# Optimization experiments

Hardware: AMD Instinct MI355X
Metric: run time of the kernel (lower is better)

## Reference

```python
import jax, jax.numpy as jnp
import numpy as np

T, B, A = 64, 512, 5
XD, YD, ZD, HD, MD = 2, 10, 16, 200, 90
HMIC, HMAC = 200, 200


def setup_inputs() -> dict:
    key = jax.random.key(0)
    ks = jax.random.split(key, 40)
    it = iter(range(40))
    def nrm(shape, s=0.05):
        return jax.random.normal(ks[next(it)], shape, jnp.float32) * s
    inp = {}
    inp["y"] = jax.random.normal(ks[next(it)], (T, B, YD), jnp.float32)
    # values in {-1} u [0, MD): -1 means "sample macro goal"
    inp["macro_goals"] = jax.random.randint(ks[next(it)], (T, B, A), 0, MD + 1, jnp.int32) - 1
    # dec_macro: Linear(YD+HMAC,HD) ReLU Linear(HD,MD) LogSoftmax
    inp["Wdm1"] = nrm((A, YD + HMAC, HD)); inp["bdm1"] = nrm((A, HD))
    inp["Wdm2"] = nrm((A, HD, MD));        inp["bdm2"] = nrm((A, MD))
    # prior: Linear(MD+HMIC,HD) ReLU Linear(HD,HD) ReLU
    inp["Wpr1"] = nrm((A, MD + HMIC, HD)); inp["bpr1"] = nrm((A, HD))
    inp["Wpr2"] = nrm((A, HD, HD));        inp["bpr2"] = nrm((A, HD))
    inp["Wpm"] = nrm((A, HD, ZD)); inp["bpm"] = nrm((A, ZD))
    inp["Wps"] = nrm((A, HD, ZD)); inp["bps"] = nrm((A, ZD))
    # dec: Linear(YD+MD+ZD+HMIC,HD) ReLU Linear(HD,HD) ReLU
    inp["Wd1"] = nrm((A, YD + MD + ZD + HMIC, HD)); inp["bd1"] = nrm((A, HD))
    inp["Wd2"] = nrm((A, HD, HD));                  inp["bd2"] = nrm((A, HD))
    inp["Wdx"] = nrm((A, HD, XD)); inp["bdx"] = nrm((A, XD))
    inp["Wds"] = nrm((A, HD, XD)); inp["bds"] = nrm((A, XD))
    # per-agent micro GRU (input XD+ZD, hidden HMIC), torch gate order [r;z;n]
    inp["Wih_mic"] = nrm((A, 3 * HMIC, XD + ZD)); inp["Whh_mic"] = nrm((A, 3 * HMIC, HMIC))
    inp["bih_mic"] = nrm((A, 3 * HMIC));          inp["bhh_mic"] = nrm((A, 3 * HMIC))
    # macro GRU (input A*MD, hidden HMAC)
    inp["Wih_mac"] = nrm((3 * HMAC, A * MD)); inp["Whh_mac"] = nrm((3 * HMAC, HMAC))
    inp["bih_mac"] = nrm((3 * HMAC,));        inp["bhh_mac"] = nrm((3 * HMAC,))
    # pre-drawn sampling noise: gumbel for multinomial, standard normal for gaussians
    u = jax.random.uniform(ks[next(it)], (T - 1, A, B, MD), jnp.float32, 1e-6, 1.0 - 1e-6)
    inp["eps_g"] = -jnp.log(-jnp.log(u))
    inp["eps_z"] = jax.random.normal(ks[next(it)], (T - 1, A, B, ZD), jnp.float32)
    inp["eps_x"] = jax.random.normal(ks[next(it)], (T - 1, A, B, XD), jnp.float32)
    inp["burn_in"] = 8
    return inp


def reference(y, Wdm1, bdm1, Wdm2, bdm2, Wpr1, bpr1, Wpr2, bpr2, Wpm, bpm, Wps, bps,
              Wd1, bd1, Wd2, bd2, Wdx, bdx, Wds, bds,
              Wih_mic, Whh_mic, bih_mic, bhh_mic, Wih_mac, Whh_mac, bih_mac, bhh_mac,
              eps_g, eps_z, eps_x, macro_goals, burn_in):
    def lin(x, W, b):  # per-agent linear: x [A,B,I], W [A,I,O]
        return jnp.einsum('abi,aio->abo', x, W) + b[:, None]

    def gru1(x, h, Wih, Whh, bih, bhh):  # x [B,I], h [B,H]
        gi = x @ Wih.T + bih
        gh = h @ Whh.T + bhh
        ir, iz, inn = jnp.split(gi, 3, -1)
        hr, hz, hn = jnp.split(gh, 3, -1)
        r = jax.nn.sigmoid(ir + hr); zg = jax.nn.sigmoid(iz + hz)
        return (1 - zg) * jnp.tanh(inn + r * hn) + zg * h

    def gruA(x, h, Wih, Whh, bih, bhh):  # x [A,B,I], h [A,B,H]
        gi = jnp.einsum('abi,agi->abg', x, Wih) + bih[:, None]
        gh = jnp.einsum('abh,agh->abg', h, Whh) + bhh[:, None]
        ir, iz, inn = jnp.split(gi, 3, -1)
        hr, hz, hn = jnp.split(gh, 3, -1)
        r = jax.nn.sigmoid(ir + hr); zg = jax.nn.sigmoid(iz + hz)
        return (1 - zg) * jnp.tanh(inn + r * hn) + zg * h

    goals_in = macro_goals[:T - 1, 0, :]  # [T-1, A]; torch code only reads batch row 0

    def step(carry, xs):
        y_t, h_mic, h_mac = carry
        t, curr, g_t, ez_t, ex_t, y_next_true = xs
        yA = jnp.broadcast_to(y_t, (A, B, YD))
        hmacA = jnp.broadcast_to(h_mac, (A, B, HMAC))
        # macro-goal decoder (log-softmax) and goal selection
        hdm = jax.nn.relu(lin(jnp.concatenate([yA, hmacA], -1), Wdm1, bdm1))
        logp = jax.nn.log_softmax(lin(hdm, Wdm2, bdm2), -1)          # [A,B,MD]
        samp_flag = (curr == -1) | ((t >= burn_in) & (burn_in > 0))  # [A]
        sampled = jax.nn.one_hot(jnp.argmax(logp + g_t, -1), MD, dtype=logp.dtype)
        fixed = jnp.zeros((A, B, MD), logp.dtype).at[:, 0, :].set(
            jax.nn.one_hot(curr, MD, dtype=logp.dtype))  # torch sets only batch row 0
        m_t = jnp.where(samp_flag[:, None, None], sampled, fixed)    # [A,B,MD]
        goals_out = jnp.argmax(m_t, -1).T                            # [B,A]
        # macro GRU over concatenated agent goals
        h_mac2 = gru1(jnp.transpose(m_t, (1, 0, 2)).reshape(B, A * MD),
                      h_mac, Wih_mac, Whh_mac, bih_mac, bhh_mac)
        # prior -> sample z
        hp = jax.nn.relu(lin(jax.nn.relu(lin(jnp.concatenate([m_t, h_mic], -1),
                                             Wpr1, bpr1)), Wpr2, bpr2))
        z_t = lin(hp, Wpm, bpm) + jax.nn.softplus(lin(hp, Wps, bps)) * ez_t  # [A,B,ZD]
        # decoder -> sample next positions (teacher-forced during burn-in)
        hd = jax.nn.relu(lin(jax.nn.relu(lin(jnp.concatenate([yA, m_t, z_t, h_mic], -1),
                                             Wd1, bd1)), Wd2, bd2))
        x_samp = lin(hd, Wdx, bdx) + jax.nn.softplus(lin(hd, Wds, bds)) * ex_t  # [A,B,XD]
        x_true = jnp.transpose(y_next_true.reshape(B, A, XD), (1, 0, 2))
        x_next = jnp.where(t < burn_in, x_true, x_samp)
        y_next = jnp.transpose(x_next, (1, 0, 2)).reshape(B, YD)
        # per-agent micro GRUs on [x_next, z]
        h_mic2 = gruA(jnp.concatenate([x_next, z_t], -1), h_mic,
                      Wih_mic, Whh_mic, bih_mic, bhh_mic)
        return (y_next, h_mic2, h_mac2), (y_next, goals_out)

    carry0 = (y[0], jnp.zeros((A, B, HMIC), y.dtype), jnp.zeros((B, HMAC), y.dtype))
    xs = (jnp.arange(T - 1), goals_in, eps_g, eps_z, eps_x, y[1:])
    _, (ys, goals) = jax.lax.scan(step, carry0, xs)
    ret = jnp.concatenate([y[:1], ys], 0)                 # [T,B,YD]
    goals_full = jnp.concatenate([goals, goals[-1:]], 0)  # [T,B,A]; last = second-last
    return ret, goals_full
```

## Files before the change

kernel.cpp:

```cpp
#include <hip/hip_runtime.h>


#define T_STEPS 63
#define BATCH   512
#define NA      5
#define YDIM    10
#define ZDIM    16
#define XDIM    2
#define HD      200
#define MDIM    90
#define HM      200
#define NB      8
#define NT      256

struct Params {
  const float *yin;
  const int   *mg;
  const float *Wdm1,*bdm1,*bdm2;
  const float *Wpr1,*bpr1,*Wpr2,*bpr2,*Wpm,*bpm,*Wps,*bps;
  const float *Wd1,*bd1,*Wd2,*bd2,*Wdx,*bdx,*Wds,*bds;
  const float *bih_mic,*bhh_mic,*bih_mac,*bhh_mac;
  const float *eps_g,*eps_z,*eps_x;
  const int   *burn;
  const float *WihTmic,*WhhTmic,*WihTmac,*WhhTmac,*Wdm2p;
  float *hmac_ws,*hmic_ws;
  int   *idxA,*idxB;
  float *ret,*goals;
};

__device__ __forceinline__ float sigm(float x){ return 1.f/(1.f+expf(-x)); }
__device__ __forceinline__ float softplusf(float x){ return log1pf(expf(-fabsf(x))) + fmaxf(x,0.f); }

template<int NBv>
__device__ __forceinline__ void mv4(const float* __restrict__ W, int N, int K,
                                    const float* __restrict__ act, int astride,
                                    int o, int kseg, float acc[4][NBv])
{
  const int Q = K >> 2;
  const int qpt = (Q + 3) >> 2;
  int q0 = kseg * qpt;
  int q1 = (Q < q0 + qpt) ? Q : (q0 + qpt);
  for (int q = q0; q < q1; ++q) {
    const float* wr = W + (size_t)(4*q)*N + o;
    const float4 w0 = *(const float4*)(wr);
    const float4 w1 = *(const float4*)(wr + N);
    const float4 w2 = *(const float4*)(wr + 2*N);
// ... 68 lines not shown
    int a = j / 10800, r = j % 10800;
    int k = r / 600, g = r % 600;
    WihTmic[j] = Wih_mic[a*10800 + g*18 + k];
  } else if (i < 1044000) {
    int j = i - 774000;
    int k = j / 600, g = j % 600;
    WihTmac[j] = Wih_mac[g*450 + k];
  } else if (i < 1140000) {
    int j = i - 1044000;
    int a = j / 19200, r = j % 19200;
    int k = r / 96, o = r % 96;
    Wdm2p[j] = (o < 90) ? Wdm2[(a*200 + k)*90 + o] : 0.f;
  }
}

__global__ __launch_bounds__(NT, 2) void step_kernel(Params p, int t)
{
  __shared__ __align__(16) float sY[NB][12];
  __shared__ __align__(16) float sHmac[NB][208];
  __shared__ __align__(16) float sHmic[NB][208];
  __shared__ __align__(16) float sGS[NB][608];
  __shared__ __align__(16) float sHn[NB][208];
  __shared__ __align__(16) float sB1[NB][208];
  __shared__ __align__(16) float sB2[NB][208];
  __shared__ __align__(16) float sLog[NB][96];
  __shared__ __align__(16) float sZ[NB][16];
  __shared__ __align__(16) float sXC[NB][20];
  __shared__ float sRedM[NB][2][8];
  __shared__ float sRedS[NB][2][8];
  __shared__ int   sIdxP[NA][NB];
  __shared__ int   sMid[NB];

  const int tid = threadIdx.x;
  const int bid = blockIdx.x;
  const int X = bid & 7, slot = bid >> 3;
  const int jj = X * 40 + slot;
  const int a  = jj >> 6;
  const int b0 = (jj & 63) * NB;
  const int burn = p.burn[0];
  const int* idxPrev = (t & 1) ? p.idxA : p.idxB;
  int*       idxCur  = (t & 1) ? p.idxB : p.idxA;

  const int og = tid >> 2;
  const int kseg = tid & 3;

  for (int u = tid; u < NB*YDIM; u += NT) {
    int j = u / YDIM, k = u % YDIM;
    float yv = (t == 0) ? p.yin[(b0+j)*YDIM + k]
                        : p.ret[(size_t)t*BATCH*YDIM + (b0+j)*YDIM + k];
    sY[j][k] = yv;
  }
  for (int u = tid; u < NB*HM; u += NT) {
    int j = u / HM, k = u % HM;
    size_t soff = ((size_t)a*BATCH + b0 + j)*HM + k;
    sHmac[j][k] = (t <= 1) ? 0.f : p.hmac_ws[soff];
    sHmic[j][k] = (t == 0) ? 0.f : p.hmic_ws[soff];
  }
  if (tid < NA*NB) {
    int a2 = tid / NB, j = tid % NB;
    sIdxP[a2][j] = (t == 0) ? -1 : idxPrev[a2*BATCH + b0 + j];
  }
  if (t == 0 && tid < NB*XDIM) {
    int j = tid >> 1, o = tid & 1;
    p.ret[(b0+j)*YDIM + a*XDIM + o] = p.yin[(b0+j)*YDIM + a*XDIM + o];
  }
  __syncthreads();

  if (t > 0) {
    #pragma unroll 1
    for (int pass = 0; pass < 3; ++pass) {
      int g4 = og + pass*64;
      if (g4 < 150) {
        int g = g4*4;
        float aI[4][NB], aH[4][NB];
        #pragma unroll
        for (int c = 0; c < 4; ++c)
          #pragma unroll
          for (int j = 0; j < NB; ++j) { aI[c][j] = 0.f; aH[c][j] = 0.f; }
        for (int a2 = kseg; a2 < NA; a2 += 4) {
          #pragma unroll
          for (int j = 0; j < NB; ++j) {
            int r = sIdxP[a2][j];
            if (r >= 0) {
              const float4 w = *(const float4*)(p.WihTmac + (size_t)(a2*MDIM + r)*600 + g);
              aI[0][j] += w.x; aI[1][j] += w.y; aI[2][j] += w.z; aI[3][j] += w.w;
            }
          }
        }
        mv4<NB>(p.WhhTmac, 600, HM, &sHmac[0][0], 208, g, kseg, aH);
        qreduce<NB>(aI);
        qreduce<NB>(aH);
        const float4 bi = *(const float4*)(p.bih_mac + g);
        const float4 bh = *(const float4*)(p.bhh_mac + g);
        #pragma unroll
        for (int j = 0; j < NB; ++j) {
          if ((j >> 1) == kseg) {
            float i0 = aI[0][j]+bi.x, i1 = aI[1][j]+bi.y, i2 = aI[2][j]+bi.z, i3 = aI[3][j]+bi.w;
            float h0 = aH[0][j]+bh.x, h1 = aH[1][j]+bh.y, h2 = aH[2][j]+bh.z, h3 = aH[3][j]+bh.w;
            if (g < 400) {
              *(float4*)&sGS[j][g] = make_float4(i0+h0, i1+h1, i2+h2, i3+h3);
            } else {
              *(float4*)&sGS[j][g] = make_float4(i0, i1, i2, i3);
              *(float4*)&sHn[j][g-400] = make_float4(h0, h1, h2, h3);
            }
          }
        }
      }
    }
    __syncthreads();
    for (int u = tid; u < NB*HM; u += NT) {
      int j = u / HM, k = u % HM;
      float r  = sigm(sGS[j][k]);
      float zg = sigm(sGS[j][200+k]);
      float nh = (1.f - zg)*tanhf(sGS[j][400+k] + r*sHn[j][k]) + zg*sHmac[j][k];
      sHmac[j][k] = nh;
      p.hmac_ws[((size_t)a*BATCH + b0 + j)*HM + k] = nh;
    }
    __syncthreads();
  }

  if (og < 50) {
    int o = og*4;
    float acc[4][NB];
    #pragma unroll
    for (int c = 0; c < 4; ++c)
      #pragma unroll
      for (int j = 0; j < NB; ++j) acc[c][j] = 0.f;
    const float* W = p.Wdm1 + (size_t)a*(YDIM+HM)*HD;
    mv4<NB>(W, HD, YDIM, &sY[0][0], 12, o, kseg, acc);
    mv4<NB>(W + (size_t)YDIM*HD, HD, HM, &sHmac[0][0], 208, o, kseg, acc);
    qreduce<NB>(acc);
    const float4 bv = *(const float4*)(p.bdm1 + a*HD + o);
    #pragma unroll
    for (int j = 0; j < NB; ++j) {
      if ((j >> 1) == kseg) {
        *(float4*)&sB1[j][o] = make_float4(
          fmaxf(acc[0][j]+bv.x, 0.f), fmaxf(acc[1][j]+bv.y, 0.f),
          fmaxf(acc[2][j]+bv.z, 0.f), fmaxf(acc[3][j]+bv.w, 0.f));
      }
    }
  }
  __syncthreads();
  if (og < 24) {
    int o = og*4;
    float acc[4][NB];
    #pragma unroll
    for (int c = 0; c < 4; ++c)
      #pragma unroll
      for (int j = 0; j < NB; ++j) acc[c][j] = 0.f;
    mv4<NB>(p.Wdm2p + (size_t)a*HD*96, 96, HD, &sB1[0][0], 208, o, kseg, acc);
    qreduce<NB>(acc);
    float b0v = (o+0 < MDIM) ? p.bdm2[a*MDIM + o+0] : 0.f;
    float b1v = (o+1 < MDIM) ? p.bdm2[a*MDIM + o+1] : 0.f;
    float b2v = (o+2 < MDIM) ? p.bdm2[a*MDIM + o+2] : 0.f;
    float b3v = (o+3 < MDIM) ? p.bdm2[a*MDIM + o+3] : 0.f;
    #pragma unroll
    for (int j = 0; j < NB; ++j) {
      if ((j >> 1) == kseg) {
        *(float4*)&sLog[j][o] = make_float4(acc[0][j]+b0v, acc[1][j]+b1v,
                                            acc[2][j]+b2v, acc[3][j]+b3v);
      }
    }
  }
  __syncthreads();
  for (int u = tid; u < NB*MDIM; u += NT) {
    int j = u / MDIM, cc = u % MDIM;
    sLog[j][cc] += p.eps_g[(((size_t)t*NA + a)*BATCH + b0 + j)*MDIM + cc];
  }
  __syncthreads();
  if (tid < NB) {
    int j = tid;
    float best = sLog[j][0]; int bi = 0;
    for (int cc = 1; cc < MDIM; ++cc) { float v = sLog[j][cc]; if (v > best) { best = v; bi = cc; } }
    int curr = p.mg[(size_t)t*BATCH*NA + a];
    bool sf = (curr == -1) || ((t >= burn) && (burn > 0));
    int mi = sf ? bi : ((b0 + j) == 0 ? curr : -1);
    sMid[j] = mi;
    float gv = (float)(mi < 0 ? 0 : mi);
    p.goals[(size_t)t*BATCH*NA + (b0+j)*NA + a] = gv;
    if (t == T_STEPS-1) p.goals[(size_t)T_STEPS*BATCH*NA + (b0+j)*NA + a] = gv;
    idxCur[a*BATCH + b0 + j] = mi;
  }
  __syncthreads();

  if (og < 50) {
    int o = og*4;
    float acc[4][NB];
    #pragma unroll
    for (int c = 0; c < 4; ++c)
      #pragma unroll
      for (int j = 0; j < NB; ++j) acc[c][j] = 0.f;
    const float* W = p.Wpr1 + (size_t)a*(MDIM+HM)*HD;
    #pragma unroll
    for (int j = 0; j < NB; ++j) {
      if ((j >> 1) == kseg) {
        int mi = sMid[j];
        if (mi >= 0) {
          const float4 w = *(const float4*)(W + (size_t)mi*HD + o);
          acc[0][j] += w.x; acc[1][j] += w.y; acc[2][j] += w.z; acc[3][j] += w.w;
        }
      }
    }
    mv4<NB>(W + (size_t)MDIM*HD, HD, HM, &sHmic[0][0], 208, o, kseg, acc);
    qreduce<NB>(acc);
    const float4 bv = *(const float4*)(p.bpr1 + a*HD + o);
    #pragma unroll
    for (int j = 0; j < NB; ++j) {
      if ((j >> 1) == kseg) {
        *(float4*)&sB2[j][o] = make_float4(
          fmaxf(acc[0][j]+bv.x, 0.f), fmaxf(acc[1][j]+bv.y, 0.f),
          fmaxf(acc[2][j]+bv.z, 0.f), fmaxf(acc[3][j]+bv.w, 0.f));
      }
    }
  }
  __syncthreads();
  if (og < 50) {
    int o = og*4;
    float acc[4][NB];
    #pragma unroll
    for (int c = 0; c < 4; ++c)
      #pragma unroll
      for (int j = 0; j < NB; ++j) acc[c][j] = 0.f;
    mv4<NB>(p.Wpr2 + (size_t)a*HD*HD, HD, HD, &sB2[0][0], 208, o, kseg, acc);
    qreduce<NB>(acc);
    const float4 bv = *(const float4*)(p.bpr2 + a*HD + o);
    #pragma unroll
    for (int j = 0; j < NB; ++j) {
      if ((j >> 1) == kseg) {
        *(float4*)&sB1[j][o] = make_float4(
          fmaxf(acc[0][j]+bv.x, 0.f), fmaxf(acc[1][j]+bv.y, 0.f),
          fmaxf(acc[2][j]+bv.z, 0.f), fmaxf(acc[3][j]+bv.w, 0.f));
      }
    }
  }
  __syncthreads();
  if (tid < NB*ZDIM) {
    int j = tid >> 4, o = tid & 15;
    float am = p.bpm[a*ZDIM + o], as = p.bps[a*ZDIM + o];
    const float* wm  = p.Wpm + (size_t)a*HD*ZDIM + o;
    const float* wsp = p.Wps + (size_t)a*HD*ZDIM + o;
    for (int k = 0; k < HD; ++k) {
      float h = sB1[j][k];
      am = fmaf(h, wm[(size_t)k*ZDIM], am);
      as = fmaf(h, wsp[(size_t)k*ZDIM], as);
    }
    float zv = am + softplusf(as) * p.eps_z[(((size_t)t*NA + a)*BATCH + b0 + j)*ZDIM + o];
    sZ[j][o] = zv;
    sXC[j][2+o] = zv;
  }
  __syncthreads();

  if (og < 50) {
    int o = og*4;
    float acc[4][NB];
    #pragma unroll
    for (int c = 0; c < 4; ++c)
      #pragma unroll
      for (int j = 0; j < NB; ++j) acc[c][j] = 0.f;
    const float* W = p.Wd1 + (size_t)a*(YDIM+MDIM+ZDIM+HM)*HD;
    #pragma unroll
    for (int j = 0; j < NB; ++j) {
      if ((j >> 1) == kseg) {
        int mi = sMid[j];
        if (mi >= 0) {
          const float4 w = *(const float4*)(W + (size_t)(YDIM+mi)*HD + o);
          acc[0][j] += w.x; acc[1][j] += w.y; acc[2][j] += w.z; acc[3][j] += w.w;
        }
      }
    }
    mv4<NB>(W, HD, YDIM, &sY[0][0], 12, o, kseg, acc);
    mv4<NB>(W + (size_t)(YDIM+MDIM)*HD, HD, ZDIM, &sZ[0][0], 16, o, kseg, acc);
    mv4<NB>(W + (size_t)(YDIM+MDIM+ZDIM)*HD, HD, HM, &sHmic[0][0], 208, o, kseg, acc);
    qreduce<NB>(acc);
    const float4 bv = *(const float4*)(p.bd1 + a*HD + o);
    #pragma unroll
    for (int j = 0; j < NB; ++j) {
      if ((j >> 1) == kseg) {
        *(float4*)&sB2[j][o] = make_float4(
          fmaxf(acc[0][j]+bv.x, 0.f), fmaxf(acc[1][j]+bv.y, 0.f),
          fmaxf(acc[2][j]+bv.z, 0.f), fmaxf(acc[3][j]+bv.w, 0.f));
      }
    }
  }
  __syncthreads();
  if (og < 50) {
    int o = og*4;
    float acc[4][NB];
    #pragma unroll
    for (int c = 0; c < 4; ++c)
      #pragma unroll
      for (int j = 0; j < NB; ++j) acc[c][j] = 0.f;
    mv4<NB>(p.Wd2 + (size_t)a*HD*HD, HD, HD, &sB2[0][0], 208, o, kseg, acc);
    qreduce<NB>(acc);
    const float4 bv = *(const float4*)(p.bd2 + a*HD + o);
    #pragma unroll
    for (int j = 0; j < NB; ++j) {
      if ((j >> 1) == kseg) {
        *(float4*)&sB1[j][o] = make_float4(
          fmaxf(acc[0][j]+bv.x, 0.f), fmaxf(acc[1][j]+bv.y, 0.f),
          fmaxf(acc[2][j]+bv.z, 0.f), fmaxf(acc[3][j]+bv.w, 0.f));
      }
    }
  }
  __syncthreads();
  if (tid < 128) {
    int j = tid >> 4, o = (tid >> 3) & 1, seg = tid & 7;
    float am = 0.f, as = 0.f;
    const float* wx  = p.Wdx + (size_t)a*HD*XDIM + o;
    const float* wsd = p.Wds + (size_t)a*HD*XDIM + o;
    for (int k = seg*25; k < seg*25 + 25; ++k) {
      float h = sB1[j][k];
      am = fmaf(h, wx[(size_t)k*XDIM], am);
      as = fmaf(h, wsd[(size_t)k*XDIM], as);
    }
    sRedM[j][o][seg] = am; sRedS[j][o][seg] = as;
  }
  __syncthreads();
  if (tid < NB*XDIM) {
    int j = tid >> 1, o = tid & 1;
    float am = p.bdx[a*XDIM + o], as = p.bds[a*XDIM + o];
    for (int s2 = 0; s2 < 8; ++s2) { am += sRedM[j][o][s2]; as += sRedS[j][o][s2]; }
    float xs = am + softplusf(as) * p.eps_x[(((size_t)t*NA + a)*BATCH + b0 + j)*XDIM + o];
    float xt = p.yin[((size_t)(t+1))*BATCH*YDIM + (b0+j)*YDIM + a*XDIM + o];
    float xv = (t < burn) ? xt : xs;
    p.ret[((size_t)(t+1))*BATCH*YDIM + (b0+j)*YDIM + a*XDIM + o] = xv;
    sXC[j][o] = xv;
  }
  __syncthreads();

  #pragma unroll 1
  for (int pass = 0; pass < 3; ++pass) {
    int g4 = og + pass*64;
    if (g4 < 150) {
      int g = g4*4;
      float aI[4][NB], aH[4][NB];
      #pragma unroll
      for (int c = 0; c < 4; ++c)
        #pragma unroll
        for (int j = 0; j < NB; ++j) { aI[c][j] = 0.f; aH[c][j] = 0.f; }
      mv4<NB>(p.WihTmic + (size_t)a*18*600, 600, 18, &sXC[0][0], 20, g, kseg, aI);
      mv4<NB>(p.WhhTmic + (size_t)a*HM*600, 600, HM, &sHmic[0][0], 208, g, kseg, aH);
      qreduce<NB>(aI);
      qreduce<NB>(aH);
      const float4 bi = *(const float4*)(p.bih_mic + a*600 + g);
      const float4 bh = *(const float4*)(p.bhh_mic + a*600 + g);
      #pragma unroll
      for (int j = 0; j < NB; ++j) {
        if ((j >> 1) == kseg) {
          float i0 = aI[0][j]+bi.x, i1 = aI[1][j]+bi.y, i2 = aI[2][j]+bi.z, i3 = aI[3][j]+bi.w;
          float h0 = aH[0][j]+bh.x, h1 = aH[1][j]+bh.y, h2 = aH[2][j]+bh.z, h3 = aH[3][j]+bh.w;
          if (g < 400) {
            *(float4*)&sGS[j][g] = make_float4(i0+h0, i1+h1, i2+h2, i3+h3);
          } else {
            *(float4*)&sGS[j][g] = make_float4(i0, i1, i2, i3);
            *(float4*)&sHn[j][g-400] = make_float4(h0, h1, h2, h3);
          }
        }
      }
    }
  }
  __syncthreads();
  for (int u = tid; u < NB*HM; u += NT) {
    int j = u / HM, k = u % HM;
    float r  = sigm(sGS[j][k]);
    float zg = sigm(sGS[j][200+k]);
    float nh = (1.f - zg)*tanhf(sGS[j][400+k] + r*sHn[j][k]) + zg*sHmic[j][k];
    p.hmic_ws[((size_t)a*BATCH + b0 + j)*HM + k] = nh;
  }
}

extern "C" void kernel_launch(void* const* d_in, const int* in_sizes, int n_in,
                              void* d_out, int out_size, void* d_ws, size_t ws_size,
                              hipStream_t stream) {
  (void)in_sizes; (void)n_in; (void)out_size; (void)ws_size;
  Params p;
  p.yin   = (const float*)d_in[0];
  p.mg    = (const int*)  d_in[1];
  p.Wdm1  = (const float*)d_in[2];  p.bdm1 = (const float*)d_in[3];
  const float* Wdm2 = (const float*)d_in[4];
  p.bdm2  = (const float*)d_in[5];
  p.Wpr1  = (const float*)d_in[6];  p.bpr1 = (const float*)d_in[7];
  p.Wpr2  = (const float*)d_in[8];  p.bpr2 = (const float*)d_in[9];
// ... 8 lines not shown
  p.bih_mic = (const float*)d_in[24]; p.bhh_mic = (const float*)d_in[25];
  const float* Wih_mac = (const float*)d_in[26];
  const float* Whh_mac = (const float*)d_in[27];
  p.bih_mac = (const float*)d_in[28]; p.bhh_mac = (const float*)d_in[29];
  p.eps_g = (const float*)d_in[30];
  p.eps_z = (const float*)d_in[31];
  p.eps_x = (const float*)d_in[32];
  p.burn  = (const int*)  d_in[33];

  float* ws = (float*)d_ws;
  float* WhhTmac = ws;
  float* WhhTmic = ws + 120000;
  float* WihTmic = ws + 720000;
  float* WihTmac = ws + 774000;
  float* Wdm2p   = ws + 1044000;
  p.hmac_ws = ws + 1140000;
  p.hmic_ws = ws + 1652000;
  int* idxbuf = (int*)(ws + 2164000);
  p.idxA = idxbuf;
  p.idxB = idxbuf + NA*BATCH;
  p.WhhTmac = WhhTmac; p.WhhTmic = WhhTmic; p.WihTmic = WihTmic; p.WihTmac = WihTmac;
  p.Wdm2p = Wdm2p;

  p.ret   = (float*)d_out;
  p.goals = (float*)d_out + (size_t)(T_STEPS+1)*BATCH*YDIM;

  prep_kernel<<<(1140000 + 255)/256, 256, 0, stream>>>(
      Whh_mac, Whh_mic, Wih_mic, Wih_mac, Wdm2,
      WhhTmac, WhhTmic, WihTmic, WihTmac, Wdm2p);

  for (int t = 0; t < T_STEPS; ++t)
    step_kernel<<<NA*64, NT, 0, stream>>>(p, t);
}
```

Measured before the change: 9.711 ms.

## Replace per-step launches with persistent cooperative kernel using flag-based inter-block sync

Turns the 63 per-timestep kernel launches into one persistent cooperative kernel. Blocks keep the GRU hidden states in shared memory across steps and exchange only macro-goal indices and sampled positions through small double-buffered global arrays. Each block waits on per-chunk acquire/release flags for just the five agent blocks of its batch chunk instead of a global barrier. It also folds the GRU reset gate into the gate computation so shared scratch can be unioned, and splits the z-head reduction across two threads. The cost is spin-waiting, and the design depends on all blocks being co-resident; if the cooperative launch fails it falls back to per-step launches.

```diff
diff --git a/kernel.cpp b/kernel.cpp
--- a/kernel.cpp
+++ b/kernel.cpp
@@ -12,6 +12,7 @@
 #define HM      200
 #define NB      8
 #define NT      256
+#define NCH     64
 
 struct Params {
   const float *yin;
@@ -23,13 +24,33 @@
   const float *eps_g,*eps_z,*eps_x;
   const int   *burn;
   const float *WihTmic,*WhhTmic,*WihTmac,*WhhTmac,*Wdm2p;
+  float *cx;
+  int   *cidx;
+  int   *fidx,*fy;
   float *hmac_ws,*hmic_ws;
-  int   *idxA,*idxB;
   float *ret,*goals;
 };
 
 __device__ __forceinline__ float sigm(float x){ return 1.f/(1.f+expf(-x)); }
 __device__ __forceinline__ float softplusf(float x){ return log1pf(expf(-fabsf(x))) + fmaxf(x,0.f); }
+__device__ __forceinline__ int ld_acq(const int* f){
+  return __hip_atomic_load(f, __ATOMIC_ACQUIRE, __HIP_MEMORY_SCOPE_AGENT);
+}
+__device__ __forceinline__ void st_rel(int* f, int v){
+  __hip_atomic_store(f, v, __ATOMIC_RELEASE, __HIP_MEMORY_SCOPE_AGENT);
+}
+__device__ __forceinline__ int ld_rlx(const int* q){
+  return __hip_atomic_load(q, __ATOMIC_RELAXED, __HIP_MEMORY_SCOPE_AGENT);
+}
+__device__ __forceinline__ float ld_rlxf(const float* q){
+  return __hip_atomic_load(q, __ATOMIC_RELAXED, __HIP_MEMORY_SCOPE_AGENT);
+}
+__device__ __forceinline__ void st_rlx(int* q, int v){
+  __hip_atomic_store(q, v, __ATOMIC_RELAXED, __HIP_MEMORY_SCOPE_AGENT);
+}
+__device__ __forceinline__ void st_rlxf(float* q, float v){
+  __hip_atomic_store(q, v, __ATOMIC_RELAXED, __HIP_MEMORY_SCOPE_AGENT);
+}
 
 template<int NBv>
 __device__ __forceinline__ void mv4(const float* __restrict__ W, int N, int K,
@@ -128,69 +149,106 @@
   }
 }
 
-__global__ __launch_bounds__(NT, 2) void step_kernel(Params p, int t)
+__global__ __launch_bounds__(NT, 2) void persist_kernel(Params p, int t0, int t1)
 {
-  __shared__ __align__(16) float sY[NB][12];
   __shared__ __align__(16) float sHmac[NB][208];
   __shared__ __align__(16) float sHmic[NB][208];
-  __shared__ __align__(16) float sGS[NB][608];
-  __shared__ __align__(16) float sHn[NB][208];
-  __shared__ __align__(16) float sB1[NB][208];
-  __shared__ __align__(16) float sB2[NB][208];
-  __shared__ __align__(16) float sLog[NB][96];
+  __shared__ __align__(16) float sXC[NB][20];
   __shared__ __align__(16) float sZ[NB][16];
-  __shared__ __align__(16) float sXC[NB][20];
   __shared__ float sRedM[NB][2][8];
   __shared__ float sRedS[NB][2][8];
-  __shared__ int   sIdxP[NA][NB];
-  __shared__ int   sMid[NB];
+  __shared__ __align__(16) union ScratchU {
+    float gs[NB][400];
+    struct { float b1[NB][208]; float b2[NB][208]; float lg[NB][96]; float y[NB][12]; } m;
+  } U;
+  __shared__ int sIdxP[NA][NB];
+  __shared__ int sMid[NB];
 
   const int tid = threadIdx.x;
   const int bid = blockIdx.x;
   const int X = bid & 7, slot = bid >> 3;
   const int jj = X * 40 + slot;
   const int a  = jj >> 6;
-  const int b0 = (jj & 63) * NB;
+  const int c  = jj & 63;
+  const int b0 = c * NB;
   const int burn = p.burn[0];
-  const int* idxPrev = (t & 1) ? p.idxA : p.idxB;
-  int*       idxCur  = (t & 1) ? p.idxB : p.idxA;
-
   const int og = tid >> 2;
   const int kseg = tid & 3;
 
-  for (int u = tid; u < NB*YDIM; u += NT) {
-    int j = u / YDIM, k = u % YDIM;
-    float yv = (t == 0) ? p.yin[(b0+j)*YDIM + k]
-                        : p.ret[(size_t)t*BATCH*YDIM + (b0+j)*YDIM + k];
-    sY[j][k] = yv;
-  }
-  for (int u = tid; u < NB*HM; u += NT) {
-    int j = u / HM, k = u % HM;
-    size_t soff = ((size_t)a*BATCH + b0 + j)*HM + k;
-    sHmac[j][k] = (t <= 1) ? 0.f : p.hmac_ws[soff];
-    sHmic[j][k] = (t == 0) ? 0.f : p.hmic_ws[soff];
-  }
-  if (tid < NA*NB) {
-    int a2 = tid / NB, j = tid % NB;
-    sIdxP[a2][j] = (t == 0) ? -1 : idxPrev[a2*BATCH + b0 + j];
-  }
-  if (t == 0 && tid < NB*XDIM) {
-    int j = tid >> 1, o = tid & 1;
-    p.ret[(b0+j)*YDIM + a*XDIM + o] = p.yin[(b0+j)*YDIM + a*XDIM + o];
+  if (t0 == 0) {
+    for (int u = tid; u < NB*HM; u += NT) {
+      int j = u / HM, k = u % HM;
+      sHmac[j][k] = 0.f; sHmic[j][k] = 0.f;
+    }
+    if (tid < NB*XDIM) {
+      int j = tid >> 1, o = tid & 1;
+      p.ret[(b0+j)*YDIM + a*XDIM + o] = p.yin[(b0+j)*YDIM + a*XDIM + o];
+    }
+  } else {
+    for (int u = tid; u < NB*HM; u += NT) {
+      int j = u / HM, k = u % HM;
+      size_t soff = ((size_t)a*BATCH + b0 + j)*HM + k;
+      sHmac[j][k] = p.hmac_ws[soff];
+      sHmic[j][k] = p.hmic_ws[soff];
+    }
   }
   __syncthreads();
 
-  if (t > 0) {
-    #pragma unroll 1
-    for (int pass = 0; pass < 3; ++pass) {
-      int g4 = og + pass*64;
-      if (g4 < 150) {
-        int g = g4*4;
+  for (int t = t0; t < t1; ++t) {
+    if (t > 0) {
+      if (tid < NA) {
+        int* f = &p.fidx[c*NA + tid];
+        while (ld_acq(f) < t) __builtin_amdgcn_s_sleep(1);
+      }
+      __syncthreads();
+      if (tid < NA*NB) {
+        int a2 = tid / NB, j = tid % NB;
+        sIdxP[a2][j] = ld_rlx(&p.cidx[((t-1)&1)*(NCH*NA*NB) + c*(NA*NB) + a2*NB + j]);
+      }
+      __syncthreads();
+      #pragma unroll 1
+      for (int pass = 0; pass < 2; ++pass) {
+        int gq = og + pass*64;
+        if (gq < 100) {
+          int g = gq*4;
+          float aI[4][NB], aH[4][NB];
+          #pragma unroll
+          for (int cc = 0; cc < 4; ++cc)
+            #pragma unroll
+            for (int j = 0; j < NB; ++j) { aI[cc][j] = 0.f; aH[cc][j] = 0.f; }
+          for (int a2 = kseg; a2 < NA; a2 += 4) {
+            #pragma unroll
+            for (int j = 0; j < NB; ++j) {
+              int r = sIdxP[a2][j];
+              if (r >= 0) {
+                const float4 w = *(const float4*)(p.WihTmac + (size_t)(a2*MDIM + r)*600 + g);
+                aI[0][j] += w.x; aI[1][j] += w.y; aI[2][j] += w.z; aI[3][j] += w.w;
+              }
+            }
+          }
+          mv4<NB>(p.WhhTmac, 600, HM, &sHmac[0][0], 208, g, kseg, aH);
+          qreduce<NB>(aI);
+          qreduce<NB>(aH);
+          const float4 bi = *(const float4*)(p.bih_mac + g);
+          const float4 bh = *(const float4*)(p.bhh_mac + g);
+          #pragma unroll
+          for (int j = 0; j < NB; ++j) {
+            if ((j >> 1) == kseg) {
+              *(float4*)&U.gs[j][g] = make_float4(aI[0][j]+bi.x+aH[0][j]+bh.x,
+                                                  aI[1][j]+bi.y+aH[1][j]+bh.y,
+                                                  aI[2][j]+bi.z+aH[2][j]+bh.z,
+                                                  aI[3][j]+bi.w+aH[3][j]+bh.w);
+            }
+          }
+        }
+      }
+      if (og < 50) {
+        int g = 400 + og*4, k4 = og*4;
         float aI[4][NB], aH[4][NB];
         #pragma unroll
-        for (int c = 0; c < 4; ++c)
+        for (int cc = 0; cc < 4; ++cc)
           #pragma unroll
-          for (int j = 0; j < NB; ++j) { aI[c][j] = 0.f; aH[c][j] = 0.f; }
+          for (int j = 0; j < NB; ++j) { aI[cc][j] = 0.f; aH[cc][j] = 0.f; }
         for (int a2 = kseg; a2 < NA; a2 += 4) {
           #pragma unroll
           for (int j = 0; j < NB; ++j) {
@@ -209,249 +267,305 @@
         #pragma unroll
         for (int j = 0; j < NB; ++j) {
           if ((j >> 1) == kseg) {
-            float i0 = aI[0][j]+bi.x, i1 = aI[1][j]+bi.y, i2 = aI[2][j]+bi.z, i3 = aI[3][j]+bi.w;
-            float h0 = aH[0][j]+bh.x, h1 = aH[1][j]+bh.y, h2 = aH[2][j]+bh.z, h3 = aH[3][j]+bh.w;
-            if (g < 400) {
-              *(float4*)&sGS[j][g] = make_float4(i0+h0, i1+h1, i2+h2, i3+h3);
-            } else {
-              *(float4*)&sGS[j][g] = make_float4(i0, i1, i2, i3);
-              *(float4*)&sHn[j][g-400] = make_float4(h0, h1, h2, h3);
-            }
+            const float4 r4 = *(const float4*)&U.gs[j][k4];
+            *(float4*)&U.gs[j][k4] = make_float4(
+              aI[0][j]+bi.x + sigm(r4.x)*(aH[0][j]+bh.x),
+              aI[1][j]+bi.y + sigm(r4.y)*(aH[1][j]+bh.y),
+              aI[2][j]+bi.z + sigm(r4.z)*(aH[2][j]+bh.z),
+              aI[3][j]+bi.w + sigm(r4.w)*(aH[3][j]+bh.w));
           }
         }
       }
-    }
-    __syncthreads();
-    for (int u = tid; u < NB*HM; u += NT) {
-      int j = u / HM, k = u % HM;
-      float r  = sigm(sGS[j][k]);
-      float zg = sigm(sGS[j][200+k]);
-      float nh = (1.f - zg)*tanhf(sGS[j][400+k] + r*sHn[j][k]) + zg*sHmac[j][k];
-      sHmac[j][k] = nh;
-      p.hmac_ws[((size_t)a*BATCH + b0 + j)*HM + k] = nh;
-    }
-    __syncthreads();
-  }
-
-  if (og < 50) {
-    int o = og*4;
-    float acc[4][NB];
-    #pragma unroll
-    for (int c = 0; c < 4; ++c)
-      #pragma unroll
-      for (int j = 0; j < NB; ++j) acc[c][j] = 0.f;
-    const float* W = p.Wdm1 + (size_t)a*(YDIM+HM)*HD;
-    mv4<NB>(W, HD, YDIM, &sY[0][0], 12, o, kseg, acc);
-    mv4<NB>(W + (size_t)YDIM*HD, HD, HM, &sHmac[0][0], 208, o, kseg, acc);
-    qreduce<NB>(acc);
-    const float4 bv = *(const float4*)(p.bdm1 + a*HD + o);
-    #pragma unroll
-    for (int j = 0; j < NB; ++j) {
-      if ((j >> 1) == kseg) {
-        *(float4*)&sB1[j][o] = make_float4(
-          fmaxf(acc[0][j]+bv.x, 0.f), fmaxf(acc[1][j]+bv.y, 0.f),
-          fmaxf(acc[2][j]+bv.z, 0.f), fmaxf(acc[3][j]+bv.w, 0.f));
-      }
-    }
-  }
-  __syncthreads();
-  if (og < 24) {
-    int o = og*4;
-    float acc[4][NB];
-    #pragma unroll
-    for (int c = 0; c < 4; ++c)
-      #pragma unroll
-      for (int j = 0; j < NB; ++j) acc[c][j] = 0.f;
-    mv4<NB>(p.Wdm2p + (size_t)a*HD*96, 96, HD, &sB1[0][0], 208, o, kseg, acc);
-    qreduce<NB>(acc);
-    float b0v = (o+0 < MDIM) ? p.bdm2[a*MDIM + o+0] : 0.f;
-    float b1v = (o+1 < MDIM) ? p.bdm2[a*MDIM + o+1] : 0.f;
-    float b2v = (o+2 < MDIM) ? p.bdm2[a*MDIM + o+2] : 0.f;
-    float b3v = (o+3 < MDIM) ? p.bdm2[a*MDIM + o+3] : 0.f;
-    #pragma unroll
-    for (int j = 0; j < NB; ++j) {
-      if ((j >> 1) == kseg) {
-        *(float4*)&sLog[j][o] = make_float4(acc[0][j]+b0v, acc[1][j]+b1v,
-                                            acc[2][j]+b2v, acc[3][j]+b3v);
-      }
-    }
-  }
-  __syncthreads();
-  for (int u = tid; u < NB*MDIM; u += NT) {
-    int j = u / MDIM, cc = u % MDIM;
-    sLog[j][cc] += p.eps_g[(((size_t)t*NA + a)*BATCH + b0 + j)*MDIM + cc];
-  }
-  __syncthreads();
-  if (tid < NB) {
-    int j = tid;
-    float best = sLog[j][0]; int bi = 0;
-    for (int cc = 1; cc < MDIM; ++cc) { float v = sLog[j][cc]; if (v > best) { best = v; bi = cc; } }
-    int curr = p.mg[(size_t)t*BATCH*NA + a];
-    bool sf = (curr == -1) || ((t >= burn) && (burn > 0));
-    int mi = sf ? bi : ((b0 + j) == 0 ? curr : -1);
-    sMid[j] = mi;
-    float gv = (float)(mi < 0 ? 0 : mi);
-    p.goals[(size_t)t*BATCH*NA + (b0+j)*NA + a] = gv;
-    if (t == T_STEPS-1) p.goals[(size_t)T_STEPS*BATCH*NA + (b0+j)*NA + a] = gv;
-    idxCur[a*BATCH + b0 + j] = mi;
-  }
-  __syncthreads();
-
-  if (og < 50) {
-    int o = og*4;
-    float acc[4][NB];
-    #pragma unroll
-    for (int c = 0; c < 4; ++c)
-      #pragma unroll
-      for (int j = 0; j < NB; ++j) acc[c][j] = 0.f;
-    const float* W = p.Wpr1 + (size_t)a*(MDIM+HM)*HD;
-    #pragma unroll
-    for (int j = 0; j < NB; ++j) {
-      if ((j >> 1) == kseg) {
-        int mi = sMid[j];
-        if (mi >= 0) {
-          const float4 w = *(const float4*)(W + (size_t)mi*HD + o);
-          acc[0][j] += w.x; acc[1][j] += w.y; acc[2][j] += w.z; acc[3][j] += w.w;
-        }
-      }
-    }
-    mv4<NB>(W + (size_t)MDIM*HD, HD, HM, &sHmic[0][0], 208, o, kseg, acc);
-    qreduce<NB>(acc);
-    const float4 bv = *(const float4*)(p.bpr1 + a*HD + o);
-    #pragma unroll
-    for (int j = 0; j < NB; ++j) {
-      if ((j >> 1) == kseg) {
-        *(float4*)&sB2[j][o] = make_float4(
-          fmaxf(acc[0][j]+bv.x, 0.f), fmaxf(acc[1][j]+bv.y, 0.f),
-          fmaxf(acc[2][j]+bv.z, 0.f), fmaxf(acc[3][j]+bv.w, 0.f));
-      }
-    }
-  }
-  __syncthreads();
-  if (og < 50) {
-    int o = og*4;
-    float acc[4][NB];
-    #pragma unroll
-    for (int c = 0; c < 4; ++c)
-      #pragma unroll
-      for (int j = 0; j < NB; ++j) acc[c][j] = 0.f;
-    mv4<NB>(p.Wpr2 + (size_t)a*HD*HD, HD, HD, &sB2[0][0], 208, o, kseg, acc);
-    qreduce<NB>(acc);
-    const float4 bv = *(const float4*)(p.bpr2 + a*HD + o);
-    #pragma unroll
-    for (int j = 0; j < NB; ++j) {
-      if ((j >> 1) == kseg) {
-        *(float4*)&sB1[j][o] = make_float4(
-          fmaxf(acc[0][j]+bv.x, 0.f), fmaxf(acc[1][j]+bv.y, 0.f),
-          fmaxf(acc[2][j]+bv.z, 0.f), fmaxf(acc[3][j]+bv.w, 0.f));
-      }
-    }
-  }
-  __syncthreads();
-  if (tid < NB*ZDIM) {
-    int j = tid >> 4, o = tid & 15;
-    float am = p.bpm[a*ZDIM + o], as = p.bps[a*ZDIM + o];
-    const float* wm  = p.Wpm + (size_t)a*HD*ZDIM + o;
-    const float* wsp = p.Wps + (size_t)a*HD*ZDIM + o;
-    for (int k = 0; k < HD; ++k) {
-      float h = sB1[j][k];
-      am = fmaf(h, wm[(size_t)k*ZDIM], am);
-      as = fmaf(h, wsp[(size_t)k*ZDIM], as);
-    }
-    float zv = am + softplusf(as) * p.eps_z[(((size_t)t*NA + a)*BATCH + b0 + j)*ZDIM + o];
-    sZ[j][o] = zv;
-    sXC[j][2+o] = zv;
-  }
-  __syncthreads();
-
-  if (og < 50) {
-    int o = og*4;
-    float acc[4][NB];
-    #pragma unroll
-    for (int c = 0; c < 4; ++c)
-      #pragma unroll
-      for (int j = 0; j < NB; ++j) acc[c][j] = 0.f;
-    const float* W = p.Wd1 + (size_t)a*(YDIM+MDIM+ZDIM+HM)*HD;
-    #pragma unroll
-    for (int j = 0; j < NB; ++j) {
-      if ((j >> 1) == kseg) {
-        int mi = sMid[j];
-        if (mi >= 0) {
-          const float4 w = *(const float4*)(W + (size_t)(YDIM+mi)*HD + o);
-          acc[0][j] += w.x; acc[1][j] += w.y; acc[2][j] += w.z; acc[3][j] += w.w;
-        }
-      }
-    }
-    mv4<NB>(W, HD, YDIM, &sY[0][0], 12, o, kseg, acc);
-    mv4<NB>(W + (size_t)(YDIM+MDIM)*HD, HD, ZDIM, &sZ[0][0], 16, o, kseg, acc);
-    mv4<NB>(W + (size_t)(YDIM+MDIM+ZDIM)*HD, HD, HM, &sHmic[0][0], 208, o, kseg, acc);
-    qreduce<NB>(acc);
-    const float4 bv = *(const float4*)(p.bd1 + a*HD + o);
-    #pragma unroll
-    for (int j = 0; j < NB; ++j) {
-      if ((j >> 1) == kseg) {
-        *(float4*)&sB2[j][o] = make_float4(
-          fmaxf(acc[0][j]+bv.x, 0.f), fmaxf(acc[1][j]+bv.y, 0.f),
-          fmaxf(acc[2][j]+bv.z, 0.f), fmaxf(acc[3][j]+bv.w, 0.f));
-      }
-    }
-  }
-  __syncthreads();
-  if (og < 50) {
-    int o = og*4;
-    float acc[4][NB];
-    #pragma unroll
-    for (int c = 0; c < 4; ++c)
-      #pragma unroll
-      for (int j = 0; j < NB; ++j) acc[c][j] = 0.f;
-    mv4<NB>(p.Wd2 + (size_t)a*HD*HD, HD, HD, &sB2[0][0], 208, o, kseg, acc);
-    qreduce<NB>(acc);
-    const float4 bv = *(const float4*)(p.bd2 + a*HD + o);
-    #pragma unroll
-    for (int j = 0; j < NB; ++j) {
-      if ((j >> 1) == kseg) {
-        *(float4*)&sB1[j][o] = make_float4(
-          fmaxf(acc[0][j]+bv.x, 0.f), fmaxf(acc[1][j]+bv.y, 0.f),
-          fmaxf(acc[2][j]+bv.z, 0.f), fmaxf(acc[3][j]+bv.w, 0.f));
-      }
-    }
-  }
-  __syncthreads();
-  if (tid < 128) {
-    int j = tid >> 4, o = (tid >> 3) & 1, seg = tid & 7;
-    float am = 0.f, as = 0.f;
-    const float* wx  = p.Wdx + (size_t)a*HD*XDIM + o;
-    const float* wsd = p.Wds + (size_t)a*HD*XDIM + o;
-    for (int k = seg*25; k < seg*25 + 25; ++k) {
-      float h = sB1[j][k];
-      am = fmaf(h, wx[(size_t)k*XDIM], am);
-      as = fmaf(h, wsd[(size_t)k*XDIM], as);
-    }
-    sRedM[j][o][seg] = am; sRedS[j][o][seg] = as;
-  }
-  __syncthreads();
-  if (tid < NB*XDIM) {
-    int j = tid >> 1, o = tid & 1;
-    float am = p.bdx[a*XDIM + o], as = p.bds[a*XDIM + o];
-    for (int s2 = 0; s2 < 8; ++s2) { am += sRedM[j][o][s2]; as += sRedS[j][o][s2]; }
-    float xs = am + softplusf(as) * p.eps_x[(((size_t)t*NA + a)*BATCH + b0 + j)*XDIM + o];
-    float xt = p.yin[((size_t)(t+1))*BATCH*YDIM + (b0+j)*YDIM + a*XDIM + o];
-    float xv = (t < burn) ? xt : xs;
-    p.ret[((size_t)(t+1))*BATCH*YDIM + (b0+j)*YDIM + a*XDIM + o] = xv;
-    sXC[j][o] = xv;
-  }
-  __syncthreads();
-
-  #pragma unroll 1
-  for (int pass = 0; pass < 3; ++pass) {
-    int g4 = og + pass*64;
-    if (g4 < 150) {
-      int g = g4*4;
+      __syncthreads();
+      for (int u = tid; u < NB*HM; u += NT) {
+        int j = u / HM, k = u % HM;
+        float zg = sigm(U.gs[j][200+k]);
+        sHmac[j][k] = (1.f - zg)*tanhf(U.gs[j][k]) + zg*sHmac[j][k];
+      }
+      __syncthreads();
+    }
+
+    if (t <= burn) {
+      for (int u = tid; u < NB*YDIM; u += NT) {
+        int j = u / YDIM, k = u % YDIM;
+        U.m.y[j][k] = p.yin[(size_t)t*BATCH*YDIM + (b0+j)*YDIM + k];
+      }
+    } else {
+      if (tid < NA) {
+        int* f = &p.fy[c*NA + tid];
+        while (ld_acq(f) < t) __builtin_amdgcn_s_sleep(1);
+      }
+      __syncthreads();
+      if (tid < NA*NB*XDIM) {
+        int a2 = tid / (NB*XDIM), r = tid % (NB*XDIM), j = r >> 1, o = r & 1;
+        U.m.y[j][a2*XDIM + o] =
+          ld_rlxf(&p.cx[((t-1)&1)*(NCH*NA*NB*XDIM) + c*(NA*NB*XDIM) + a2*(NB*XDIM) + j*XDIM + o]);
+      }
+    }
+    __syncthreads();
+
+    if (og < 50) {
+      int o = og*4;
+      float acc[4][NB];
+      #pragma unroll
+      for (int cc = 0; cc < 4; ++cc)
+        #pragma unroll
+        for (int j = 0; j < NB; ++j) acc[cc][j] = 0.f;
+      const float* W = p.Wdm1 + (size_t)a*(YDIM+HM)*HD;
+      mv4<NB>(W, HD, YDIM, &U.m.y[0][0], 12, o, kseg, acc);
+      mv4<NB>(W + (size_t)YDIM*HD, HD, HM, &sHmac[0][0], 208, o, kseg, acc);
+      qreduce<NB>(acc);
+      const float4 bv = *(const float4*)(p.bdm1 + a*HD + o);
+      #pragma unroll
+      for (int j = 0; j < NB; ++j) {
+        if ((j >> 1) == kseg) {
+          *(float4*)&U.m.b1[j][o] = make_float4(
+            fmaxf(acc[0][j]+bv.x, 0.f), fmaxf(acc[1][j]+bv.y, 0.f),
+            fmaxf(acc[2][j]+bv.z, 0.f), fmaxf(acc[3][j]+bv.w, 0.f));
+        }
+      }
+    }
+    __syncthreads();
+    if (og < 24) {
+      int o = og*4;
+      float acc[4][NB];
+      #pragma unroll
+      for (int cc = 0; cc < 4; ++cc)
+        #pragma unroll
+        for (int j = 0; j < NB; ++j) acc[cc][j] = 0.f;
+      mv4<NB>(p.Wdm2p + (size_t)a*HD*96, 96, HD, &U.m.b1[0][0], 208, o, kseg, acc);
+      qreduce<NB>(acc);
+      float b0v = (o+0 < MDIM) ? p.bdm2[a*MDIM + o+0] : 0.f;
+      float b1v = (o+1 < MDIM) ? p.bdm2[a*MDIM + o+1] : 0.f;
+      float b2v = (o+2 < MDIM) ? p.bdm2[a*MDIM + o+2] : 0.f;
+      float b3v = (o+3 < MDIM) ? p.bdm2[a*MDIM + o+3] : 0.f;
+      #pragma unroll
+      for (int j = 0; j < NB; ++j) {
+        if ((j >> 1) == kseg) {
+          *(float4*)&U.m.lg[j][o] = make_float4(acc[0][j]+b0v, acc[1][j]+b1v,
+                                                acc[2][j]+b2v, acc[3][j]+b3v);
+        }
+      }
+    }
+    __syncthreads();
+    for (int u = tid; u < NB*MDIM; u += NT) {
+      int j = u / MDIM, cc = u % MDIM;
+      U.m.lg[j][cc] += p.eps_g[(((size_t)t*NA + a)*BATCH + b0 + j)*MDIM + cc];
+    }
+    __syncthreads();
+    if (tid < 64) {
+      int j = tid >> 3, s = tid & 7;
+      float best = -3.4e38f; int bi2 = 0;
+      for (int cc = s; cc < MDIM; cc += 8) {
+        float v = U.m.lg[j][cc];
+        if (v > best) { best = v; bi2 = cc; }
+      }
+      #pragma unroll
+      for (int d = 1; d < 8; d <<= 1) {
+        float ob = __shfl_xor(best, d); int oi = __shfl_xor(bi2, d);
+        if (ob > best || (ob == best && oi < bi2)) { best = ob; bi2 = oi; }
+      }
+      if (s == 0) {
+        int curr = p.mg[(size_t)t*BATCH*NA + a];
+        bool sf = (curr == -1) || ((t >= burn) && (burn > 0));
+        int mi = sf ? bi2 : ((b0 + j) == 0 ? curr : -1);
+        sMid[j] = mi;
+        float gv = (float)(mi < 0 ? 0 : mi);
+        p.goals[(size_t)t*BATCH*NA + (b0+j)*NA + a] = gv;
+        if (t == T_STEPS-1) p.goals[(size_t)T_STEPS*BATCH*NA + (b0+j)*NA + a] = gv;
+        st_rlx(&p.cidx[(t&1)*(NCH*NA*NB) + c*(NA*NB) + a*NB + j], mi);
+      }
+    }
+    __syncthreads();
+    if (tid == 0) { __threadfence(); st_rel(&p.fidx[c*NA + a], t+1); }
+
+    if (og < 50) {
+      int o = og*4;
+      float acc[4][NB];
+      #pragma unroll
+      for (int cc = 0; cc < 4; ++cc)
+        #pragma unroll
+        for (int j = 0; j < NB; ++j) acc[cc][j] = 0.f;
+      const float* W = p.Wpr1 + (size_t)a*(MDIM+HM)*HD;
+      #pragma unroll
+      for (int j = 0; j < NB; ++j) {
+        if ((j >> 1) == kseg) {
+          int mi = sMid[j];
+          if (mi >= 0) {
+            const float4 w = *(const float4*)(W + (size_t)mi*HD + o);
+            acc[0][j] += w.x; acc[1][j] += w.y; acc[2][j] += w.z; acc[3][j] += w.w;
+          }
+        }
+      }
+      mv4<NB>(W + (size_t)MDIM*HD, HD, HM, &sHmic[0][0], 208, o, kseg, acc);
+      qreduce<NB>(acc);
+      const float4 bv = *(const float4*)(p.bpr1 + a*HD + o);
+      #pragma unroll
+      for (int j = 0; j < NB; ++j) {
+        if ((j >> 1) == kseg) {
+          *(float4*)&U.m.b2[j][o] = make_float4(
+            fmaxf(acc[0][j]+bv.x, 0.f), fmaxf(acc[1][j]+bv.y, 0.f),
+            fmaxf(acc[2][j]+bv.z, 0.f), fmaxf(acc[3][j]+bv.w, 0.f));
+        }
+      }
+    }
+    __syncthreads();
+    if (og < 50) {
+      int o = og*4;
+      float acc[4][NB];
+      #pragma unroll
+      for (int cc = 0; cc < 4; ++cc)
+        #pragma unroll
+        for (int j = 0; j < NB; ++j) acc[cc][j] = 0.f;
+      mv4<NB>(p.Wpr2 + (size_t)a*HD*HD, HD, HD, &U.m.b2[0][0], 208, o, kseg, acc);
+      qreduce<NB>(acc);
+      const float4 bv = *(const float4*)(p.bpr2 + a*HD + o);
+      #pragma unroll
+      for (int j = 0; j < NB; ++j) {
+        if ((j >> 1) == kseg) {
+          *(float4*)&U.m.b1[j][o] = make_float4(
+            fmaxf(acc[0][j]+bv.x, 0.f), fmaxf(acc[1][j]+bv.y, 0.f),
+            fmaxf(acc[2][j]+bv.z, 0.f), fmaxf(acc[3][j]+bv.w, 0.f));
+        }
+      }
+    }
+    __syncthreads();
+    {
+      int j = tid >> 5, o = (tid >> 1) & 15, s = tid & 1;
+      float am = 0.f, as = 0.f;
+      const float* wm  = p.Wpm + (size_t)a*HD*ZDIM + o;
+      const float* wsp = p.Wps + (size_t)a*HD*ZDIM + o;
+      for (int k = s*100; k < s*100 + 100; ++k) {
+        float h = U.m.b1[j][k];
+        am = fmaf(h, wm[(size_t)k*ZDIM], am);
+        as = fmaf(h, wsp[(size_t)k*ZDIM], as);
+      }
+      am += __shfl_xor(am, 1);
+      as += __shfl_xor(as, 1);
+      if (s == 0) {
+        am += p.bpm[a*ZDIM + o];
+        as += p.bps[a*ZDIM + o];
+        float zv = am + softplusf(as) * p.eps_z[(((size_t)t*NA + a)*BATCH + b0 + j)*ZDIM + o];
+        sZ[j][o] = zv;
+        sXC[j][2+o] = zv;
+      }
+    }
+    __syncthreads();
+
+    if (og < 50) {
+      int o = og*4;
+      float acc[4][NB];
+      #pragma unroll
+      for (int cc = 0; cc < 4; ++cc)
+        #pragma unroll
+        for (int j = 0; j < NB; ++j) acc[cc][j] = 0.f;
+      const float* W = p.Wd1 + (size_t)a*(YDIM+MDIM+ZDIM+HM)*HD;
+      #pragma unroll
+      for (int j = 0; j < NB; ++j) {
+        if ((j >> 1) == kseg) {
+          int mi = sMid[j];
+          if (mi >= 0) {
+            const float4 w = *(const float4*)(W + (size_t)(YDIM+mi)*HD + o);
+            acc[0][j] += w.x; acc[1][j] += w.y; acc[2][j] += w.z; acc[3][j] += w.w;
+          }
+        }
+      }
+      mv4<NB>(W, HD, YDIM, &U.m.y[0][0], 12, o, kseg, acc);
+      mv4<NB>(W + (size_t)(YDIM+MDIM)*HD, HD, ZDIM, &sZ[0][0], 16, o, kseg, acc);
+      mv4<NB>(W + (size_t)(YDIM+MDIM+ZDIM)*HD, HD, HM, &sHmic[0][0], 208, o, kseg, acc);
+      qreduce<NB>(acc);
+      const float4 bv = *(const float4*)(p.bd1 + a*HD + o);
+      #pragma unroll
+      for (int j = 0; j < NB; ++j) {
+        if ((j >> 1) == kseg) {
+          *(float4*)&U.m.b2[j][o] = make_float4(
+            fmaxf(acc[0][j]+bv.x, 0.f), fmaxf(acc[1][j]+bv.y, 0.f),
+            fmaxf(acc[2][j]+bv.z, 0.f), fmaxf(acc[3][j]+bv.w, 0.f));
+        }
+      }
+    }
+    __syncthreads();
+    if (og < 50) {
+      int o = og*4;
+      float acc[4][NB];
+      #pragma unroll
+      for (int cc = 0; cc < 4; ++cc)
+        #pragma unroll
+        for (int j = 0; j < NB; ++j) acc[cc][j] = 0.f;
+      mv4<NB>(p.Wd2 + (size_t)a*HD*HD, HD, HD, &U.m.b2[0][0], 208, o, kseg, acc);
+      qreduce<NB>(acc);
+      const float4 bv = *(const float4*)(p.bd2 + a*HD + o);
+      #pragma unroll
+      for (int j = 0; j < NB; ++j) {
+        if ((j >> 1) == kseg) {
+          *(float4*)&U.m.b1[j][o] = make_float4(
+            fmaxf(acc[0][j]+bv.x, 0.f), fmaxf(acc[1][j]+bv.y, 0.f),
+            fmaxf(acc[2][j]+bv.z, 0.f), fmaxf(acc[3][j]+bv.w, 0.f));
+        }
+      }
+    }
+    __syncthreads();
+    if (tid < 128) {
+      int j = tid >> 4, o = (tid >> 3) & 1, seg = tid & 7;
+      float am = 0.f, as = 0.f;
+      const float* wx  = p.Wdx + (size_t)a*HD*XDIM + o;
+      const float* wsd = p.Wds + (size_t)a*HD*XDIM + o;
+      for (int k = seg*25; k < seg*25 + 25; ++k) {
+        float h = U.m.b1[j][k];
+        am = fmaf(h, wx[(size_t)k*XDIM], am);
+        as = fmaf(h, wsd[(size_t)k*XDIM], as);
+      }
+      sRedM[j][o][seg] = am; sRedS[j][o][seg] = as;
+    }
+    __syncthreads();
+    if (tid < NB*XDIM) {
+      int j = tid >> 1, o = tid & 1;
+      float am = p.bdx[a*XDIM + o], as = p.bds[a*XDIM + o];
+      for (int s2 = 0; s2 < 8; ++s2) { am += sRedM[j][o][s2]; as += sRedS[j][o][s2]; }
+      float xs = am + softplusf(as) * p.eps_x[(((size_t)t*NA + a)*BATCH + b0 + j)*XDIM + o];
+      float xt = p.yin[((size_t)(t+1))*BATCH*YDIM + (b0+j)*YDIM + a*XDIM + o];
+      float xv = (t < burn) ? xt : xs;
+      p.ret[((size_t)(t+1))*BATCH*YDIM + (b0+j)*YDIM + a*XDIM + o] = xv;
+      st_rlxf(&p.cx[(t&1)*(NCH*NA*NB*XDIM) + c*(NA*NB*XDIM) + a*(NB*XDIM) + j*XDIM + o], xv);
+      sXC[j][o] = xv;
+    }
+    __syncthreads();
+    if (tid == 0) { __threadfence(); st_rel(&p.fy[c*NA + a], t+1); }
+
+    #pragma unroll 1
+    for (int pass = 0; pass < 2; ++pass) {
+      int gq = og + pass*64;
+      if (gq < 100) {
+        int g = gq*4;
+        float aI[4][NB], aH[4][NB];
+        #pragma unroll
+        for (int cc = 0; cc < 4; ++cc)
+          #pragma unroll
+          for (int j = 0; j < NB; ++j) { aI[cc][j] = 0.f; aH[cc][j] = 0.f; }
+        mv4<NB>(p.WihTmic + (size_t)a*18*600, 600, 18, &sXC[0][0], 20, g, kseg, aI);
+        mv4<NB>(p.WhhTmic + (size_t)a*HM*600, 600, HM, &sHmic[0][0], 208, g, kseg, aH);
+        qreduce<NB>(aI);
+        qreduce<NB>(aH);
+        const float4 bi = *(const float4*)(p.bih_mic + a*600 + g);
+        const float4 bh = *(const float4*)(p.bhh_mic + a*600 + g);
+        #pragma unroll
+        for (int j = 0; j < NB; ++j) {
+          if ((j >> 1) == kseg) {
+            *(float4*)&U.gs[j][g] = make_float4(aI[0][j]+bi.x+aH[0][j]+bh.x,
+                                                aI[1][j]+bi.y+aH[1][j]+bh.y,
+                                                aI[2][j]+bi.z+aH[2][j]+bh.z,
+                                                aI[3][j]+bi.w+aH[3][j]+bh.w);
+          }
+        }
+      }
+    }
+    if (og < 50) {
+      int g = 400 + og*4, k4 = og*4;
       float aI[4][NB], aH[4][NB];
       #pragma unroll
-      for (int c = 0; c < 4; ++c)
-        #pragma unroll
-        for (int j = 0; j < NB; ++j) { aI[c][j] = 0.f; aH[c][j] = 0.f; }
+      for (int cc = 0; cc < 4; ++cc)
+        #pragma unroll
+        for (int j = 0; j < NB; ++j) { aI[cc][j] = 0.f; aH[cc][j] = 0.f; }
       mv4<NB>(p.WihTmic + (size_t)a*18*600, 600, 18, &sXC[0][0], 20, g, kseg, aI);
       mv4<NB>(p.WhhTmic + (size_t)a*HM*600, 600, HM, &sHmic[0][0], 208, g, kseg, aH);
       qreduce<NB>(aI);
@@ -461,25 +575,29 @@
       #pragma unroll
       for (int j = 0; j < NB; ++j) {
         if ((j >> 1) == kseg) {
-          float i0 = aI[0][j]+bi.x, i1 = aI[1][j]+bi.y, i2 = aI[2][j]+bi.z, i3 = aI[3][j]+bi.w;
-          float h0 = aH[0][j]+bh.x, h1 = aH[1][j]+bh.y, h2 = aH[2][j]+bh.z, h3 = aH[3][j]+bh.w;
-          if (g < 400) {
-            *(float4*)&sGS[j][g] = make_float4(i0+h0, i1+h1, i2+h2, i3+h3);
-          } else {
-            *(float4*)&sGS[j][g] = make_float4(i0, i1, i2, i3);
-            *(float4*)&sHn[j][g-400] = make_float4(h0, h1, h2, h3);
-          }
-        }
-      }
-    }
-  }
-  __syncthreads();
+          const float4 r4 = *(const float4*)&U.gs[j][k4];
+          *(float4*)&U.gs[j][k4] = make_float4(
+            aI[0][j]+bi.x + sigm(r4.x)*(aH[0][j]+bh.x),
+            aI[1][j]+bi.y + sigm(r4.y)*(aH[1][j]+bh.y),
+            aI[2][j]+bi.z + sigm(r4.z)*(aH[2][j]+bh.z),
+            aI[3][j]+bi.w + sigm(r4.w)*(aH[3][j]+bh.w));
+        }
+      }
+    }
+    __syncthreads();
+    for (int u = tid; u < NB*HM; u += NT) {
+      int j = u / HM, k = u % HM;
+      float zg = sigm(U.gs[j][200+k]);
+      sHmic[j][k] = (1.f - zg)*tanhf(U.gs[j][k]) + zg*sHmic[j][k];
+    }
+    __syncthreads();
+  }
+
   for (int u = tid; u < NB*HM; u += NT) {
     int j = u / HM, k = u % HM;
-    float r  = sigm(sGS[j][k]);
-    float zg = sigm(sGS[j][200+k]);
-    float nh = (1.f - zg)*tanhf(sGS[j][400+k] + r*sHn[j][k]) + zg*sHmic[j][k];
-    p.hmic_ws[((size_t)a*BATCH + b0 + j)*HM + k] = nh;
+    size_t soff = ((size_t)a*BATCH + b0 + j)*HM + k;
+    p.hmac_ws[soff] = sHmac[j][k];
+    p.hmic_ws[soff] = sHmic[j][k];
   }
 }
 
@@ -518,11 +636,12 @@
   float* WihTmic = ws + 720000;
   float* WihTmac = ws + 774000;
   float* Wdm2p   = ws + 1044000;
-  p.hmac_ws = ws + 1140000;
-  p.hmic_ws = ws + 1652000;
-  int* idxbuf = (int*)(ws + 2164000);
-  p.idxA = idxbuf;
-  p.idxB = idxbuf + NA*BATCH;
+  p.cx   = ws + 1140000;
+  p.cidx = (int*)(ws + 1150240);
+  p.fidx = p.cidx + 5120;
+  p.fy   = p.fidx + 320;
+  p.hmac_ws = ws + 1156000;
+  p.hmic_ws = ws + 1668000;
   p.WhhTmac = WhhTmac; p.WhhTmic = WhhTmic; p.WihTmic = WihTmic; p.WihTmac = WihTmac;
   p.Wdm2p = Wdm2p;
 
@@ -532,7 +651,20 @@
   prep_kernel<<<(1140000 + 255)/256, 256, 0, stream>>>(
       Whh_mac, Whh_mic, Wih_mic, Wih_mac, Wdm2,
       WhhTmac, WhhTmic, WihTmic, WihTmac, Wdm2p);
-
-  for (int t = 0; t < T_STEPS; ++t)
-    step_kernel<<<NA*64, NT, 0, stream>>>(p, t);
-}
+  hipMemsetAsync((void*)p.fidx, 0, 640*sizeof(int), stream);
+
+  int maxb = 0;
+  hipError_t qe = hipOccupancyMaxActiveBlocksPerMultiprocessor(&maxb, persist_kernel, NT, 0);
+  bool coop = (qe == hipSuccess) && (maxb >= 2);
+  if (coop) {
+    int t0 = 0, t1 = T_STEPS;
+    void* args[] = { (void*)&p, (void*)&t0, (void*)&t1 };
+    hipError_t rc = hipLaunchCooperativeKernel((const void*)persist_kernel,
+                                               dim3(NA*NCH), dim3(NT), args, 0, stream);
+    if (rc != hipSuccess) coop = false;
+  }
+  if (!coop) {
+    for (int t = 0; t < T_STEPS; ++t)
+      persist_kernel<<<NA*NCH, NT, 0, stream>>>(p, t, t+1);
+  }
+}
```

New measurement: 14.74 ms. +51.7%, slower.
